# Kernel optimization log

Measured on AMD Instinct MI355X. Metric: run time of the kernel, lower is better.

## Reference

```python
import jax, jax.numpy as jnp
import numpy as np

B, D, H = 1024, 64, 512


def setup_inputs() -> dict:
    key = jax.random.key(0)
    ks = jax.random.split(key, 6)
    sc = lambda fan_in: 1.0 / np.sqrt(fan_in)
    return {
        "x_t": jax.random.normal(ks[0], (B, D), jnp.float32),
        "t": jax.random.uniform(ks[1], (B, 1), dtype=jnp.float32),
        "beta": jax.random.uniform(ks[2], (B, 1), dtype=jnp.float32),
        "W1": jax.random.normal(ks[3], (D + 1, H), jnp.float32) * sc(D + 1),
        "b1": jnp.zeros((H,), jnp.float32),
        "W2": jax.random.normal(ks[4], (H, H), jnp.float32) * sc(H),
        "b2": jnp.zeros((H,), jnp.float32),
        "W3": jax.random.normal(ks[5], (H, D), jnp.float32) * sc(H),
        "b3": jnp.zeros((D,), jnp.float32),
    }


def _score(W1, b1, W2, b2, W3, b3, x, t):
    # x: [D], t: [1] -> s: [D]; small tanh MLP score network s(x, t)
    h = jnp.tanh(jnp.concatenate([x, t]) @ W1 + b1)
    h = jnp.tanh(h @ W2 + b2)
    return h @ W3 + b3


def reference(x_t, t, beta, W1, b1, W2, b2, W3, b3):
    def per_sample(x, tt):
        s_x = lambda xx: _score(W1, b1, W2, b2, W3, b3, xx, tt)
        s_t_fn = lambda ttt: _score(W1, b1, W2, b2, W3, b3, x, ttt)

        # s_t = grad(sum(s), t): sum over output dims of ds/dt (forward-mode JVP)
        _, s_dot = jax.jvp(s_t_fn, (tt,), (jnp.ones_like(tt),))
        s_t = jnp.sum(s_dot)  # scalar per sample

        # phi(x) = div_x s + |s|^2 + <s, x>; loss term = grad_x phi (2nd order through div)
        def phi(xx):
            jac = jax.jacfwd(s_x)(xx)          # [D, D]
            div = jnp.trace(jac)
            s = s_x(xx)
            return div + jnp.sum(s * s) + jnp.dot(s, xx)

        g = jax.grad(phi)(x)  # [D]
        return s_t, g

    s_t, g = jax.vmap(per_sample)(x_t, t)  # s_t: [B], g: [B, D]
    # loss = mean_D |s_t - 0.5 * beta * grad|, shape [B, 1]
    return jnp.mean(jnp.abs(s_t[:, None] - 0.5 * beta * g), axis=1, keepdims=True)
```

## Files before the change

### kernel.cpp

```cpp
#include <hip/hip_runtime.h>
#include <math.h>


#define Bsz 1024
#define Dd  64
#define Hh  512

__global__ __launch_bounds__(256) void kpre(const float* __restrict__ W1,
                                            const float* __restrict__ W3,
                                            const float* __restrict__ W2,
                                            float* __restrict__ C,
                                            float* __restrict__ w3sum) {
  const int b = blockIdx.x;
  const int tid = threadIdx.x;
  if (b < 64) {
    __shared__ float W1s[64][68];
    __shared__ float W3s[64][68];
    const int bj = (b & 7) * 64, bl = (b >> 3) * 64;
    for (int q = 0; q < 16; q++) {
      int idx = tid + q * 256;
      int i = idx >> 6, j = idx & 63;
      W1s[i][j] = W1[i * Hh + bj + j];
    }
    for (int q = 0; q < 16; q++) {
      int idx = tid + q * 256;
      int l = idx >> 6, i = idx & 63;
      W3s[i][l] = W3[(bl + l) * Dd + i];
    }
    __syncthreads();
    const int tj = (tid >> 4) << 2, tl = (tid & 15) << 2;
    float acc[4][4] = {};
#pragma unroll 8
    for (int i = 0; i < 64; i++) {
      float4 a = *(const float4*)&W1s[i][tj];
      float4 bb = *(const float4*)&W3s[i][tl];
      float ar[4] = {a.x, a.y, a.z, a.w};
      float br[4] = {bb.x, bb.y, bb.z, bb.w};
#pragma unroll
      for (int r = 0; r < 4; r++)
#pragma unroll
        for (int c = 0; c < 4; c++) acc[r][c] += ar[r] * br[c];
    }
#pragma unroll
    for (int r = 0; r < 4; r++) {
      int j = bj + tj + r;
      float4 cv;
#pragma unroll
      for (int c = 0; c < 4; c++)
        ((float*)&cv)[c] = W2[j * Hh + bl + tl + c] * acc[r][c];
      *(float4*)&C[j * Hh + bl + tl] = cv;
    }
  } else {
#pragma unroll
    for (int r = 0; r < 2; r++) {
      int n = tid + r * 256;
      float sacc = 0.f;
#pragma unroll 4
      for (int k4 = 0; k4 < 16; k4++) {
        float4 w = *(const float4*)&W3[n * Dd + k4 * 4];
        sacc += w.x; sacc += w.y; sacc += w.z; sacc += w.w;
      }
      w3sum[n] = sacc;
    }
  }
}

__global__ __launch_bounds__(512) void kfused(const float* __restrict__ X,
                                              const float* __restrict__ tt,
                                              const float* __restrict__ beta,
                                              const float* __restrict__ W1,
                                              const float* __restrict__ b1,
                                              const float* __restrict__ W2,
                                              const float* __restrict__ b2,
                                              const float* __restrict__ W3,
                                              const float* __restrict__ b3,
                                              const float* __restrict__ C,
                                              const float* __restrict__ w3sum,
                                              float* __restrict__ out) {
  __shared__ float xs[Dd * 4], ys[Dd * 4];
  __shared__ float h1s[Hh * 4], a1s[Hh * 4], q1s[Hh * 4];
  __shared__ float h2s[Hh * 4], a2s[Hh * 4], t2s[Hh * 4], ps[Hh * 4];
  __shared__ float sts[4], tb[4], bb4[4], red[32];
  __shared__ float ph[512];

  const int tid = threadIdx.x;
  const int s0 = blockIdx.x * 4;
  const int n0 = tid;
  const int dd = tid & 63;
  const int half = (tid >> 6) & 1;
  const int ss = tid >> 7;

  if (tid < 256) {
    int sA = tid >> 6, dA = tid & 63;
    xs[dA * 4 + sA] = X[(s0 + sA) * Dd + dA];
  }
  if (tid < 4) tb[tid] = tt[s0 + tid];
  else if (tid < 8) bb4[tid - 4] = beta[s0 + tid - 4];
  __syncthreads();

  {
    float acc[4] = {};
#pragma unroll 8
    for (int k = 0; k < Dd; k++) {
      float w = W1[k * Hh + n0];
      float4 xv = *(const float4*)&xs[k * 4];
#pragma unroll
      for (int s = 0; s < 4; s++) acc[s] += w * ((float*)&xv)[s];
    }
    float wt = W1[Dd * Hh + n0];
    float bc = b1[n0];
    float4 hv, av, qv;
#pragma unroll
    for (int s = 0; s < 4; s++) {
      float z = acc[s] + tb[s] * wt + bc;
      float h = tanhf(z);
      float a = 1.f - h * h;
      ((float*)&hv)[s] = h;
      ((float*)&av)[s] = a;
      ((float*)&qv)[s] = a * wt;
    }
    *(float4*)&h1s[n0 * 4] = hv;
    *(float4*)&a1s[n0 * 4] = av;
    *(float4*)&q1s[n0 * 4] = qv;
  }
  __syncthreads();

  {
    float acc1[4] = {}, acc2[4] = {};
#pragma unroll 8
    for (int k = 0; k < Hh; k++) {
      float w = W2[k * Hh + n0];
      float4 hv = *(const float4*)&h1s[k * 4];
      float4 qv = *(const float4*)&q1s[k * 4];
#pragma unroll
      for (int s = 0; s < 4; s++) {
        acc1[s] += w * ((float*)&hv)[s];
        acc2[s] += w * ((float*)&qv)[s];
      }
    }
    float bc = b2[n0], wc = w3sum[n0];
    float stp[4];
    float4 hv, av;
#pragma unroll
    for (int s = 0; s < 4; s++) {
      float z = acc1[s] + bc;
      float h = tanhf(z);
      float a = 1.f - h * h;
      ((float*)&hv)[s] = h;
      ((float*)&av)[s] = a;
      stp[s] = a * acc2[s] * wc;
    }
    *(float4*)&h2s[n0 * 4] = hv;
    *(float4*)&a2s[n0 * 4] = av;
#pragma unroll
    for (int off = 1; off < 64; off <<= 1)
#pragma unroll
      for (int s = 0; s < 4; s++) stp[s] += __shfl_xor(stp[s], off, 64);
    if (dd == 0)
#pragma unroll
      for (int s = 0; s < 4; s++) red[(tid >> 6) * 4 + s] = stp[s];
  }
  __syncthreads();
  if (tid < 4) {
    float t = 0.f;
#pragma unroll
    for (int w = 0; w < 8; w++) t += red[w * 4 + tid];
    sts[tid] = t;
  }

  {
    float sacc = half ? 0.f : b3[dd];
    const int l0 = half * 256;
#pragma unroll 8
    for (int l = l0; l < l0 + 256; l++)
      sacc += W3[l * Dd + dd] * h2s[l * 4 + ss];
    ph[tid] = sacc;
  }
  __syncthreads();
  float sval = 0.f;
  if (half == 0) {
    sval = ph[ss * 128 + dd] + ph[ss * 128 + 64 + dd];
    ys[dd * 4 + ss] = 2.f * sval + xs[dd * 4 + ss];
  }
  __syncthreads();

  float ua[4] = {};
  {
    float r3a[4] = {};
#pragma unroll 4
    for (int k4 = 0; k4 < 16; k4++) {
      float4 w = *(const float4*)&W3[n0 * Dd + k4 * 4];
#pragma unroll
      for (int j = 0; j < 4; j++) {
        float4 yv = *(const float4*)&ys[(k4 * 4 + j) * 4];
#pragma unroll
        for (int s = 0; s < 4; s++) r3a[s] += ((float*)&w)[j] * ((float*)&yv)[s];
      }
    }
    float va[4] = {};
#pragma unroll 2
    for (int k4 = 0; k4 < 128; k4++) {
      float4 cu = *(const float4*)&C[n0 * Hh + k4 * 4];
#pragma unroll
      for (int j = 0; j < 4; j++) {
        int k = k4 * 4 + j;
        float cv = C[k * Hh + n0];
        float4 a1v = *(const float4*)&a1s[k * 4];
        float4 a2v = *(const float4*)&a2s[k * 4];
#pragma unroll
        for (int s = 0; s < 4; s++) {
          va[s] += cv * ((float*)&a1v)[s];
          ua[s] += ((float*)&cu)[j] * ((float*)&a2v)[s];
        }
      }
    }
    float4 a2r = *(const float4*)&a2s[n0 * 4];
    float4 h2r = *(const float4*)&h2s[n0 * 4];
    float4 t2v;
#pragma unroll
    for (int s = 0; s < 4; s++)
      ((float*)&t2v)[s] = ((float*)&a2r)[s] *
          (r3a[s] - 2.f * ((float*)&h2r)[s] * va[s]);
    *(float4*)&t2s[n0 * 4] = t2v;
  }
  __syncthreads();

  {
    float pa[4] = {};
#pragma unroll 2
    for (int k4 = 0; k4 < 128; k4++) {
      float4 w = *(const float4*)&W2[n0 * Hh + k4 * 4];
#pragma unroll
      for (int j = 0; j < 4; j++) {
        float4 t2v = *(const float4*)&t2s[(k4 * 4 + j) * 4];
#pragma unroll
        for (int s = 0; s < 4; s++) pa[s] += ((float*)&w)[j] * ((float*)&t2v)[s];
      }
    }
    float4 a1r = *(const float4*)&a1s[n0 * 4];
    float4 h1r = *(const float4*)&h1s[n0 * 4];
    float4 pv;
#pragma unroll
    for (int s = 0; s < 4; s++)
      ((float*)&pv)[s] = ((float*)&a1r)[s] *
          (pa[s] - 2.f * ((float*)&h1r)[s] * ua[s]);
    *(float4*)&ps[n0 * 4] = pv;
  }
  __syncthreads();

  {
    float g = (half == 0) ? sval : 0.f;
    const int j0 = half * 256;
#pragma unroll 4
    for (int j4 = 0; j4 < 64; j4++) {
      float4 w = *(const float4*)&W1[dd * Hh + j0 + j4 * 4];
#pragma unroll
      for (int j = 0; j < 4; j++)
        g += ((float*)&w)[j] * ps[(j0 + j4 * 4 + j) * 4 + ss];
    }
    ph[tid] = g;
  }
  __syncthreads();
  if (half == 0) {
    float g = ph[ss * 128 + dd] + ph[ss * 128 + 64 + dd];
    float e = fabsf(sts[ss] - 0.5f * bb4[ss] * g);
#pragma unroll
    for (int off = 32; off; off >>= 1) e += __shfl_down(e, off, 64);
    if (dd == 0) out[s0 + ss] = e * (1.f / 64.f);
  }
}

extern "C" void kernel_launch(void* const* d_in, const int* in_sizes, int n_in,
                              void* d_out, int out_size, void* d_ws, size_t ws_size,
                              hipStream_t stream) {
  const float* X    = (const float*)d_in[0];
  const float* tt   = (const float*)d_in[1];
  const float* beta = (const float*)d_in[2];
  const float* W1   = (const float*)d_in[3];
  const float* b1   = (const float*)d_in[4];
  const float* W2   = (const float*)d_in[5];
  const float* b2   = (const float*)d_in[6];
  const float* W3   = (const float*)d_in[7];
  const float* b3   = (const float*)d_in[8];
  float* out = (float*)d_out;

  float* ws  = (float*)d_ws;
  float* C   = ws;
  float* w3s = C + 262144;

  kpre<<<65, 256, 0, stream>>>(W1, W3, W2, C, w3s);
  kfused<<<256, 512, 0, stream>>>(X, tt, beta, W1, b1, W2, b2, W3, b3, C, w3s, out);
}
```

Baseline: 199.1 us.

## Pretranspose weights for row-contiguous float4 loads and halve samples per block

The precompute kernel now also writes transposed copies of C, W2, W1 and W3 into workspace. This lets every matvec in the fused kernel read a contiguous row per thread with float4 loads instead of strided column loads. The fused kernel handles 2 samples per block instead of 4, doubling the grid to 512 blocks with a higher occupancy hint. The trade-off is more workspace traffic in the precompute, and each weight byte is reused across fewer samples, so total weight reads double.

```diff
diff --git a/kernel.cpp b/kernel.cpp
--- a/kernel.cpp
+++ b/kernel.cpp
@@ -2,38 +2,40 @@
 #include <math.h>
 
 
-#define Bsz 1024
-#define Dd  64
-#define Hh  512
+#define Dd 64
+#define Hh 512
+#define S  2
 
 __global__ __launch_bounds__(256) void kpre(const float* __restrict__ W1,
                                             const float* __restrict__ W3,
                                             const float* __restrict__ W2,
                                             float* __restrict__ C,
+                                            float* __restrict__ CT,
+                                            float* __restrict__ W2T,
+                                            float* __restrict__ W1T,
+                                            float* __restrict__ W3T,
                                             float* __restrict__ w3sum) {
-  const int b = blockIdx.x;
-  const int tid = threadIdx.x;
+  const int b = blockIdx.x, tid = threadIdx.x;
+  __shared__ float sA[64][68];
+  __shared__ float sB[64][68];
+  __shared__ float sT[64][65];
   if (b < 64) {
-    __shared__ float W1s[64][68];
-    __shared__ float W3s[64][68];
     const int bj = (b & 7) * 64, bl = (b >> 3) * 64;
     for (int q = 0; q < 16; q++) {
-      int idx = tid + q * 256;
-      int i = idx >> 6, j = idx & 63;
-      W1s[i][j] = W1[i * Hh + bj + j];
-    }
-    for (int q = 0; q < 16; q++) {
-      int idx = tid + q * 256;
-      int l = idx >> 6, i = idx & 63;
-      W3s[i][l] = W3[(bl + l) * Dd + i];
+      int idx = tid + q * 256, i = idx >> 6, j = idx & 63;
+      sA[i][j] = W1[i * Hh + bj + j];
+    }
+    for (int q = 0; q < 16; q++) {
+      int idx = tid + q * 256, l = idx >> 6, i = idx & 63;
+      sB[i][l] = W3[(bl + l) * Dd + i];
     }
     __syncthreads();
     const int tj = (tid >> 4) << 2, tl = (tid & 15) << 2;
     float acc[4][4] = {};
 #pragma unroll 8
     for (int i = 0; i < 64; i++) {
-      float4 a = *(const float4*)&W1s[i][tj];
-      float4 bb = *(const float4*)&W3s[i][tl];
+      float4 a = *(const float4*)&sA[i][tj];
+      float4 bb = *(const float4*)&sB[i][tl];
       float ar[4] = {a.x, a.y, a.z, a.w};
       float br[4] = {bb.x, bb.y, bb.z, bb.w};
 #pragma unroll
@@ -41,14 +43,54 @@
 #pragma unroll
         for (int c = 0; c < 4; c++) acc[r][c] += ar[r] * br[c];
     }
+    float cv[4][4];
+#pragma unroll
+    for (int r = 0; r < 4; r++)
+#pragma unroll
+      for (int c = 0; c < 4; c++)
+        cv[r][c] = W2[(bj + tj + r) * Hh + bl + tl + c] * acc[r][c];
 #pragma unroll
     for (int r = 0; r < 4; r++) {
-      int j = bj + tj + r;
-      float4 cv;
-#pragma unroll
-      for (int c = 0; c < 4; c++)
-        ((float*)&cv)[c] = W2[j * Hh + bl + tl + c] * acc[r][c];
-      *(float4*)&C[j * Hh + bl + tl] = cv;
+      float4 o = {cv[r][0], cv[r][1], cv[r][2], cv[r][3]};
+      *(float4*)&C[(bj + tj + r) * Hh + bl + tl] = o;
+    }
+#pragma unroll
+    for (int c = 0; c < 4; c++) {
+      float4 o = {cv[0][c], cv[1][c], cv[2][c], cv[3][c]};
+      *(float4*)&CT[(bl + tl + c) * Hh + bj + tj] = o;
+    }
+  } else if (b < 128) {
+    const int t = b - 64, r0 = (t & 7) * 64, c0 = (t >> 3) * 64;
+    for (int q = 0; q < 16; q++) {
+      int idx = tid + q * 256, i = idx >> 6, j = idx & 63;
+      sT[i][j] = W2[(r0 + i) * Hh + c0 + j];
+    }
+    __syncthreads();
+    for (int q = 0; q < 16; q++) {
+      int idx = tid + q * 256, i = idx >> 6, j = idx & 63;
+      W2T[(c0 + i) * Hh + r0 + j] = sT[j][i];
+    }
+  } else if (b < 136) {
+    const int t = b - 128, c0 = t * 64;
+    for (int q = 0; q < 16; q++) {
+      int idx = tid + q * 256, i = idx >> 6, j = idx & 63;
+      sT[i][j] = W1[i * Hh + c0 + j];
+    }
+    __syncthreads();
+    for (int q = 0; q < 16; q++) {
+      int idx = tid + q * 256, i = idx >> 6, j = idx & 63;
+      W1T[(c0 + i) * Dd + j] = sT[j][i];
+    }
+  } else if (b < 144) {
+    const int t = b - 136, r0 = t * 64;
+    for (int q = 0; q < 16; q++) {
+      int idx = tid + q * 256, i = idx >> 6, j = idx & 63;
+      sT[i][j] = W3[(r0 + i) * Dd + j];
+    }
+    __syncthreads();
+    for (int q = 0; q < 16; q++) {
+      int idx = tid + q * 256, i = idx >> 6, j = idx & 63;
+      W3T[i * Hh + r0 + j] = sT[j][i];
     }
   } else {
 #pragma unroll
@@ -65,208 +107,242 @@
   }
 }
 
-__global__ __launch_bounds__(512) void kfused(const float* __restrict__ X,
-                                              const float* __restrict__ tt,
-                                              const float* __restrict__ beta,
-                                              const float* __restrict__ W1,
-                                              const float* __restrict__ b1,
-                                              const float* __restrict__ W2,
-                                              const float* __restrict__ b2,
-                                              const float* __restrict__ W3,
-                                              const float* __restrict__ b3,
-                                              const float* __restrict__ C,
-                                              const float* __restrict__ w3sum,
-                                              float* __restrict__ out) {
-  __shared__ float xs[Dd * 4], ys[Dd * 4];
-  __shared__ float h1s[Hh * 4], a1s[Hh * 4], q1s[Hh * 4];
-  __shared__ float h2s[Hh * 4], a2s[Hh * 4], t2s[Hh * 4], ps[Hh * 4];
-  __shared__ float sts[4], tb[4], bb4[4], red[32];
+__global__ __launch_bounds__(512, 4) void kfused(const float* __restrict__ X,
+                                                 const float* __restrict__ tt,
+                                                 const float* __restrict__ beta,
+                                                 const float* __restrict__ W1,
+                                                 const float* __restrict__ b1,
+                                                 const float* __restrict__ W2,
+                                                 const float* __restrict__ b2,
+                                                 const float* __restrict__ W3,
+                                                 const float* __restrict__ b3,
+                                                 const float* __restrict__ C,
+                                                 const float* __restrict__ CT,
+                                                 const float* __restrict__ W2T,
+                                                 const float* __restrict__ W1T,
+                                                 const float* __restrict__ W3T,
+                                                 const float* __restrict__ w3sum,
+                                                 float* __restrict__ out) {
+  __shared__ float xs[Dd * S], ys[Dd * S];
+  __shared__ float h1s[Hh * S], a1s[Hh * S], q1s[Hh * S];
+  __shared__ float h2s[Hh * S], a2s[Hh * S], t2s[Hh * S], ps[Hh * S];
+  __shared__ float sts[S], tb[S], bbv[S], red[8 * S];
   __shared__ float ph[512];
 
   const int tid = threadIdx.x;
-  const int s0 = blockIdx.x * 4;
+  const int s0 = blockIdx.x * S;
   const int n0 = tid;
-  const int dd = tid & 63;
-  const int half = (tid >> 6) & 1;
-  const int ss = tid >> 7;
-
-  if (tid < 256) {
+  const int ssD = tid >> 8;
+  const int qqD = (tid >> 6) & 3;
+  const int ddD = tid & 63;
+
+  if (tid < Dd * S) {
     int sA = tid >> 6, dA = tid & 63;
-    xs[dA * 4 + sA] = X[(s0 + sA) * Dd + dA];
-  }
-  if (tid < 4) tb[tid] = tt[s0 + tid];
-  else if (tid < 8) bb4[tid - 4] = beta[s0 + tid - 4];
-  __syncthreads();
-
-  {
-    float acc[4] = {};
-#pragma unroll 8
-    for (int k = 0; k < Dd; k++) {
-      float w = W1[k * Hh + n0];
-      float4 xv = *(const float4*)&xs[k * 4];
-#pragma unroll
-      for (int s = 0; s < 4; s++) acc[s] += w * ((float*)&xv)[s];
-    }
-    float wt = W1[Dd * Hh + n0];
-    float bc = b1[n0];
-    float4 hv, av, qv;
-#pragma unroll
-    for (int s = 0; s < 4; s++) {
+    xs[dA * S + sA] = X[(s0 + sA) * Dd + dA];
+  }
+  if (tid < S) tb[tid] = tt[s0 + tid];
+  if (tid >= 64 && tid < 64 + S) bbv[tid - 64] = beta[s0 + tid - 64];
+  __syncthreads();
+
+  {
+    float acc[S] = {};
+    for (int k0 = 0; k0 < Dd; k0 += 32) {
+      float4 wv[8];
+#pragma unroll
+      for (int i = 0; i < 8; i++) wv[i] = *(const float4*)&W1T[n0 * Dd + k0 + i * 4];
+#pragma unroll
+      for (int i = 0; i < 8; i++)
+#pragma unroll
+        for (int j = 0; j < 4; j++) {
+          float w = ((float*)&wv[i])[j];
+          float2 xv = *(const float2*)&xs[(k0 + i * 4 + j) * S];
+          acc[0] += w * xv.x; acc[1] += w * xv.y;
+        }
+    }
+    float wt = W1[Dd * Hh + n0], bc = b1[n0];
+    float2 hv, av, qv;
+#pragma unroll
+    for (int s = 0; s < S; s++) {
       float z = acc[s] + tb[s] * wt + bc;
       float h = tanhf(z);
       float a = 1.f - h * h;
-      ((float*)&hv)[s] = h;
-      ((float*)&av)[s] = a;
-      ((float*)&qv)[s] = a * wt;
-    }
-    *(float4*)&h1s[n0 * 4] = hv;
-    *(float4*)&a1s[n0 * 4] = av;
-    *(float4*)&q1s[n0 * 4] = qv;
-  }
-  __syncthreads();
-
-  {
-    float acc1[4] = {}, acc2[4] = {};
-#pragma unroll 8
-    for (int k = 0; k < Hh; k++) {
-      float w = W2[k * Hh + n0];
-      float4 hv = *(const float4*)&h1s[k * 4];
-      float4 qv = *(const float4*)&q1s[k * 4];
-#pragma unroll
-      for (int s = 0; s < 4; s++) {
-        acc1[s] += w * ((float*)&hv)[s];
-        acc2[s] += w * ((float*)&qv)[s];
-      }
+      ((float*)&hv)[s] = h; ((float*)&av)[s] = a; ((float*)&qv)[s] = a * wt;
+    }
+    *(float2*)&h1s[n0 * S] = hv;
+    *(float2*)&a1s[n0 * S] = av;
+    *(float2*)&q1s[n0 * S] = qv;
+  }
+  __syncthreads();
+
+  {
+    float acc1[S] = {}, acc2[S] = {};
+    for (int k0 = 0; k0 < Hh; k0 += 32) {
+      float4 wv[8];
+#pragma unroll
+      for (int i = 0; i < 8; i++) wv[i] = *(const float4*)&W2T[n0 * Hh + k0 + i * 4];
+#pragma unroll
+      for (int i = 0; i < 8; i++)
+#pragma unroll
+        for (int j = 0; j < 4; j++) {
+          int k = k0 + i * 4 + j;
+          float w = ((float*)&wv[i])[j];
+          float2 hv = *(const float2*)&h1s[k * S];
+          float2 qv = *(const float2*)&q1s[k * S];
+          acc1[0] += w * hv.x; acc1[1] += w * hv.y;
+          acc2[0] += w * qv.x; acc2[1] += w * qv.y;
+        }
     }
     float bc = b2[n0], wc = w3sum[n0];
-    float stp[4];
-    float4 hv, av;
-#pragma unroll
-    for (int s = 0; s < 4; s++) {
+    float stp[S];
+    float2 hv, av;
+#pragma unroll
+    for (int s = 0; s < S; s++) {
       float z = acc1[s] + bc;
       float h = tanhf(z);
       float a = 1.f - h * h;
-      ((float*)&hv)[s] = h;
-      ((float*)&av)[s] = a;
+      ((float*)&hv)[s] = h; ((float*)&av)[s] = a;
       stp[s] = a * acc2[s] * wc;
     }
-    *(float4*)&h2s[n0 * 4] = hv;
-    *(float4*)&a2s[n0 * 4] = av;
+    *(float2*)&h2s[n0 * S] = hv;
+    *(float2*)&a2s[n0 * S] = av;
 #pragma unroll
     for (int off = 1; off < 64; off <<= 1)
 #pragma unroll
-      for (int s = 0; s < 4; s++) stp[s] += __shfl_xor(stp[s], off, 64);
-    if (dd == 0)
-#pragma unroll
-      for (int s = 0; s < 4; s++) red[(tid >> 6) * 4 + s] = stp[s];
-  }
-  __syncthreads();
-  if (tid < 4) {
+      for (int s = 0; s < S; s++) stp[s] += __shfl_xor(stp[s], off, 64);
+    if ((tid & 63) == 0)
+#pragma unroll
+      for (int s = 0; s < S; s++) red[(tid >> 6) * S + s] = stp[s];
+  }
+  __syncthreads();
+  if (tid < S) {
     float t = 0.f;
 #pragma unroll
-    for (int w = 0; w < 8; w++) t += red[w * 4 + tid];
+    for (int w = 0; w < 8; w++) t += red[w * S + tid];
     sts[tid] = t;
   }
 
   {
-    float sacc = half ? 0.f : b3[dd];
-    const int l0 = half * 256;
-#pragma unroll 8
-    for (int l = l0; l < l0 + 256; l++)
-      sacc += W3[l * Dd + dd] * h2s[l * 4 + ss];
+    float sacc = (qqD == 0) ? b3[ddD] : 0.f;
+    const int l0 = qqD * 128;
+    for (int c0 = 0; c0 < 128; c0 += 32) {
+      float4 wv[8];
+#pragma unroll
+      for (int i = 0; i < 8; i++) wv[i] = *(const float4*)&W3T[ddD * Hh + l0 + c0 + i * 4];
+#pragma unroll
+      for (int i = 0; i < 8; i++)
+#pragma unroll
+        for (int j = 0; j < 4; j++)
+          sacc += ((float*)&wv[i])[j] * h2s[(l0 + c0 + i * 4 + j) * S + ssD];
+    }
     ph[tid] = sacc;
   }
   __syncthreads();
   float sval = 0.f;
-  if (half == 0) {
-    sval = ph[ss * 128 + dd] + ph[ss * 128 + 64 + dd];
-    ys[dd * 4 + ss] = 2.f * sval + xs[dd * 4 + ss];
-  }
-  __syncthreads();
-
-  float ua[4] = {};
-  {
-    float r3a[4] = {};
-#pragma unroll 4
-    for (int k4 = 0; k4 < 16; k4++) {
-      float4 w = *(const float4*)&W3[n0 * Dd + k4 * 4];
-#pragma unroll
-      for (int j = 0; j < 4; j++) {
-        float4 yv = *(const float4*)&ys[(k4 * 4 + j) * 4];
-#pragma unroll
-        for (int s = 0; s < 4; s++) r3a[s] += ((float*)&w)[j] * ((float*)&yv)[s];
+  if (tid < 128) {
+    int ssf = tid >> 6, ddf = tid & 63;
+    sval = ph[ssf * 256 + ddf];
+    sval += ph[ssf * 256 + 64 + ddf];
+    sval += ph[ssf * 256 + 128 + ddf];
+    sval += ph[ssf * 256 + 192 + ddf];
+    ys[ddf * S + ssf] = 2.f * sval + xs[ddf * S + ssf];
+  }
+  __syncthreads();
+
+  float ua[S] = {};
+  {
+    float r3a[S] = {};
+    for (int k0 = 0; k0 < Dd; k0 += 32) {
+      float4 wv[8];
+#pragma unroll
+      for (int i = 0; i < 8; i++) wv[i] = *(const float4*)&W3[n0 * Dd + k0 + i * 4];
+#pragma unroll
+      for (int i = 0; i < 8; i++)
+#pragma unroll
+        for (int j = 0; j < 4; j++) {
+          float w = ((float*)&wv[i])[j];
+          float2 yv = *(const float2*)&ys[(k0 + i * 4 + j) * S];
+          r3a[0] += w * yv.x; r3a[1] += w * yv.y;
+        }
+    }
+    float va[S] = {};
+    for (int k0 = 0; k0 < Hh; k0 += 16) {
+      float4 cu[4], cw[4];
+#pragma unroll
+      for (int i = 0; i < 4; i++) {
+        cu[i] = *(const float4*)&C[n0 * Hh + k0 + i * 4];
+        cw[i] = *(const float4*)&CT[n0 * Hh + k0 + i * 4];
       }
-    }
-    float va[4] = {};
-#pragma unroll 2
-    for (int k4 = 0; k4 < 128; k4++) {
-      float4 cu = *(const float4*)&C[n0 * Hh + k4 * 4];
-#pragma unroll
-      for (int j = 0; j < 4; j++) {
-        int k = k4 * 4 + j;
-        float cv = C[k * Hh + n0];
-        float4 a1v = *(const float4*)&a1s[k * 4];
-        float4 a2v = *(const float4*)&a2s[k * 4];
-#pragma unroll
-        for (int s = 0; s < 4; s++) {
-          va[s] += cv * ((float*)&a1v)[s];
-          ua[s] += ((float*)&cu)[j] * ((float*)&a2v)[s];
-        }
-      }
-    }
-    float4 a2r = *(const float4*)&a2s[n0 * 4];
-    float4 h2r = *(const float4*)&h2s[n0 * 4];
-    float4 t2v;
-#pragma unroll
-    for (int s = 0; s < 4; s++)
-      ((float*)&t2v)[s] = ((float*)&a2r)[s] *
-          (r3a[s] - 2.f * ((float*)&h2r)[s] * va[s]);
-    *(float4*)&t2s[n0 * 4] = t2v;
-  }
-  __syncthreads();
-
-  {
-    float pa[4] = {};
-#pragma unroll 2
-    for (int k4 = 0; k4 < 128; k4++) {
-      float4 w = *(const float4*)&W2[n0 * Hh + k4 * 4];
-#pragma unroll
-      for (int j = 0; j < 4; j++) {
-        float4 t2v = *(const float4*)&t2s[(k4 * 4 + j) * 4];
-#pragma unroll
-        for (int s = 0; s < 4; s++) pa[s] += ((float*)&w)[j] * ((float*)&t2v)[s];
-      }
-    }
-    float4 a1r = *(const float4*)&a1s[n0 * 4];
-    float4 h1r = *(const float4*)&h1s[n0 * 4];
-    float4 pv;
-#pragma unroll
-    for (int s = 0; s < 4; s++)
-      ((float*)&pv)[s] = ((float*)&a1r)[s] *
-          (pa[s] - 2.f * ((float*)&h1r)[s] * ua[s]);
-    *(float4*)&ps[n0 * 4] = pv;
-  }
-  __syncthreads();
-
-  {
-    float g = (half == 0) ? sval : 0.f;
-    const int j0 = half * 256;
-#pragma unroll 4
-    for (int j4 = 0; j4 < 64; j4++) {
-      float4 w = *(const float4*)&W1[dd * Hh + j0 + j4 * 4];
-#pragma unroll
-      for (int j = 0; j < 4; j++)
-        g += ((float*)&w)[j] * ps[(j0 + j4 * 4 + j) * 4 + ss];
-    }
-    ph[tid] = g;
-  }
-  __syncthreads();
-  if (half == 0) {
-    float g = ph[ss * 128 + dd] + ph[ss * 128 + 64 + dd];
-    float e = fabsf(sts[ss] - 0.5f * bb4[ss] * g);
+#pragma unroll
+      for (int i = 0; i < 4; i++)
+#pragma unroll
+        for (int j = 0; j < 4; j++) {
+          int k = k0 + i * 4 + j;
+          float2 a1v = *(const float2*)&a1s[k * S];
+          float2 a2v = *(const float2*)&a2s[k * S];
+          float u_ = ((float*)&cu[i])[j], v_ = ((float*)&cw[i])[j];
+          va[0] += v_ * a1v.x; va[1] += v_ * a1v.y;
+          ua[0] += u_ * a2v.x; ua[1] += u_ * a2v.y;
+        }
+    }
+    float2 a2r = *(const float2*)&a2s[n0 * S];
+    float2 h2r = *(const float2*)&h2s[n0 * S];
+    float2 t2v;
+    t2v.x = a2r.x * (r3a[0] - 2.f * h2r.x * va[0]);
+    t2v.y = a2r.y * (r3a[1] - 2.f * h2r.y * va[1]);
+    *(float2*)&t2s[n0 * S] = t2v;
+  }
+  __syncthreads();
+
+  {
+    float pa[S] = {};
+    for (int k0 = 0; k0 < Hh; k0 += 32) {
+      float4 wv[8];
+#pragma unroll
+      for (int i = 0; i < 8; i++) wv[i] = *(const float4*)&W2[n0 * Hh + k0 + i * 4];
+#pragma unroll
+      for (int i = 0; i < 8; i++)
+#pragma unroll
+        for (int j = 0; j < 4; j++) {
+          float w = ((float*)&wv[i])[j];
+          float2 tv = *(const float2*)&t2s[(k0 + i * 4 + j) * S];
+          pa[0] += w * tv.x; pa[1] += w * tv.y;
+        }
+    }
+    float2 a1r = *(const float2*)&a1s[n0 * S];
+    float2 h1r = *(const float2*)&h1s[n0 * S];
+    float2 pv;
+    pv.x = a1r.x * (pa[0] - 2.f * h1r.x * ua[0]);
+    pv.y = a1r.y * (pa[1] - 2.f * h1r.y * ua[1]);
+    *(float2*)&ps[n0 * S] = pv;
+  }
+  __syncthreads();
+
+  {
+    float gq = 0.f;
+    const int j0 = qqD * 128;
+    for (int c0 = 0; c0 < 128; c0 += 32) {
+      float4 wv[8];
+#pragma unroll
+      for (int i = 0; i < 8; i++) wv[i] = *(const float4*)&W1[ddD * Hh + j0 + c0 + i * 4];
+#pragma unroll
+      for (int i = 0; i < 8; i++)
+#pragma unroll
+        for (int j = 0; j < 4; j++)
+          gq += ((float*)&wv[i])[j] * ps[(j0 + c0 + i * 4 + j) * S + ssD];
+    }
+    ph[tid] = gq;
+  }
+  __syncthreads();
+  if (tid < 128) {
+    int ssf = tid >> 6, ddf = tid & 63;
+    float g = sval + ph[ssf * 256 + ddf];
+    g += ph[ssf * 256 + 64 + ddf];
+    g += ph[ssf * 256 + 128 + ddf];
+    g += ph[ssf * 256 + 192 + ddf];
+    float e = fabsf(sts[ssf] - 0.5f * bbv[ssf] * g);
 #pragma unroll
     for (int off = 32; off; off >>= 1) e += __shfl_down(e, off, 64);
-    if (dd == 0) out[s0 + ss] = e * (1.f / 64.f);
+    if (ddf == 0) out[s0 + ssf] = e * (1.f / 64.f);
   }
 }
 
@@ -284,10 +360,15 @@
   const float* b3   = (const float*)d_in[8];
   float* out = (float*)d_out;
 
-  float* ws  = (float*)d_ws;
-  float* C   = ws;
-  float* w3s = C + 262144;
-
-  kpre<<<65, 256, 0, stream>>>(W1, W3, W2, C, w3s);
-  kfused<<<256, 512, 0, stream>>>(X, tt, beta, W1, b1, W2, b2, W3, b3, C, w3s, out);
+  float* ws   = (float*)d_ws;
+  float* C    = ws;
+  float* CT   = C + 262144;
+  float* W2T  = CT + 262144;
+  float* W1T  = W2T + 262144;
+  float* W3T  = W1T + 32768;
+  float* w3s  = W3T + 32768;
+
+  kpre<<<145, 256, 0, stream>>>(W1, W3, W2, C, CT, W2T, W1T, W3T, w3s);
+  kfused<<<512, 512, 0, stream>>>(X, tt, beta, W1, b1, W2, b2, W3, b3,
+                                  C, CT, W2T, W1T, W3T, w3s, out);
 }
```

Result: slower. 392.9 us (+97.3%).

## Pre-transpose weights so fused kernel reads contiguous float4 rows per thread

Applied to the files above, without the earlier changes.

The preprocessing kernel now also writes transposed copies of C, W2, W1 and W3 into workspace. The fused kernel then reads each thread's weight row with contiguous float4 loads instead of strided scalar column loads, using macro-unrolled FMA chains. This trades coalesced scalar loads across threads for per-thread vector loads, and adds extra transpose work and workspace traffic in kpre.

```diff
diff --git a/kernel.cpp b/kernel.cpp
--- a/kernel.cpp
+++ b/kernel.cpp
@@ -2,38 +2,39 @@
 #include <math.h>
 
 
-#define Bsz 1024
-#define Dd  64
-#define Hh  512
+#define Dd 64
+#define Hh 512
 
 __global__ __launch_bounds__(256) void kpre(const float* __restrict__ W1,
                                             const float* __restrict__ W3,
                                             const float* __restrict__ W2,
                                             float* __restrict__ C,
+                                            float* __restrict__ CT,
+                                            float* __restrict__ W2T,
+                                            float* __restrict__ W1T,
+                                            float* __restrict__ W3T,
                                             float* __restrict__ w3sum) {
-  const int b = blockIdx.x;
-  const int tid = threadIdx.x;
+  const int b = blockIdx.x, tid = threadIdx.x;
+  __shared__ float sA[64][68];
+  __shared__ float sB[64][68];
+  __shared__ float sT[64][65];
   if (b < 64) {
-    __shared__ float W1s[64][68];
-    __shared__ float W3s[64][68];
     const int bj = (b & 7) * 64, bl = (b >> 3) * 64;
     for (int q = 0; q < 16; q++) {
-      int idx = tid + q * 256;
-      int i = idx >> 6, j = idx & 63;
-      W1s[i][j] = W1[i * Hh + bj + j];
-    }
-    for (int q = 0; q < 16; q++) {
-      int idx = tid + q * 256;
-      int l = idx >> 6, i = idx & 63;
-      W3s[i][l] = W3[(bl + l) * Dd + i];
+      int idx = tid + q * 256, i = idx >> 6, j = idx & 63;
+      sA[i][j] = W1[i * Hh + bj + j];
+    }
+    for (int q = 0; q < 16; q++) {
+      int idx = tid + q * 256, l = idx >> 6, i = idx & 63;
+      sB[i][l] = W3[(bl + l) * Dd + i];
     }
     __syncthreads();
     const int tj = (tid >> 4) << 2, tl = (tid & 15) << 2;
     float acc[4][4] = {};
 #pragma unroll 8
     for (int i = 0; i < 64; i++) {
-      float4 a = *(const float4*)&W1s[i][tj];
-      float4 bb = *(const float4*)&W3s[i][tl];
+      float4 a = *(const float4*)&sA[i][tj];
+      float4 bb = *(const float4*)&sB[i][tl];
       float ar[4] = {a.x, a.y, a.z, a.w};
       float br[4] = {bb.x, bb.y, bb.z, bb.w};
 #pragma unroll
@@ -41,14 +42,54 @@
 #pragma unroll
         for (int c = 0; c < 4; c++) acc[r][c] += ar[r] * br[c];
     }
+    float cv[4][4];
+#pragma unroll
+    for (int r = 0; r < 4; r++)
+#pragma unroll
+      for (int c = 0; c < 4; c++)
+        cv[r][c] = W2[(bj + tj + r) * Hh + bl + tl + c] * acc[r][c];
 #pragma unroll
     for (int r = 0; r < 4; r++) {
-      int j = bj + tj + r;
-      float4 cv;
-#pragma unroll
-      for (int c = 0; c < 4; c++)
-        ((float*)&cv)[c] = W2[j * Hh + bl + tl + c] * acc[r][c];
-      *(float4*)&C[j * Hh + bl + tl] = cv;
+      float4 o = {cv[r][0], cv[r][1], cv[r][2], cv[r][3]};
+      *(float4*)&C[(bj + tj + r) * Hh + bl + tl] = o;
+    }
+#pragma unroll
+    for (int c = 0; c < 4; c++) {
+      float4 o = {cv[0][c], cv[1][c], cv[2][c], cv[3][c]};
+      *(float4*)&CT[(bl + tl + c) * Hh + bj + tj] = o;
+    }
+  } else if (b < 128) {
+    const int t = b - 64, r0 = (t & 7) * 64, c0 = (t >> 3) * 64;
+    for (int q = 0; q < 16; q++) {
+      int idx = tid + q * 256, i = idx >> 6, j = idx & 63;
+      sT[i][j] = W2[(r0 + i) * Hh + c0 + j];
+    }
+    __syncthreads();
+    for (int q = 0; q < 16; q++) {
+      int idx = tid + q * 256, i = idx >> 6, j = idx & 63;
+      W2T[(c0 + i) * Hh + r0 + j] = sT[j][i];
+    }
+  } else if (b < 136) {
+    const int t = b - 128, c0 = t * 64;
+    for (int q = 0; q < 16; q++) {
+      int idx = tid + q * 256, i = idx >> 6, j = idx & 63;
+      sT[i][j] = W1[i * Hh + c0 + j];
+    }
+    __syncthreads();
+    for (int q = 0; q < 16; q++) {
+      int idx = tid + q * 256, i = idx >> 6, j = idx & 63;
+      W1T[(c0 + i) * Dd + j] = sT[j][i];
+    }
+  } else if (b < 144) {
+    const int t = b - 136, r0 = t * 64;
+    for (int q = 0; q < 16; q++) {
+      int idx = tid + q * 256, i = idx >> 6, j = idx & 63;
+      sT[i][j] = W3[(r0 + i) * Dd + j];
+    }
+    __syncthreads();
+    for (int q = 0; q < 16; q++) {
+      int idx = tid + q * 256, i = idx >> 6, j = idx & 63;
+      W3T[i * Hh + r0 + j] = sT[j][i];
     }
   } else {
 #pragma unroll
@@ -64,6 +105,18 @@
     }
   }
 }
+
+#define LD4(P, kb)                                   \
+  float4 w0 = *(const float4*)&(P)[(kb)];            \
+  float4 w1 = *(const float4*)&(P)[(kb) + 4];        \
+  float4 w2 = *(const float4*)&(P)[(kb) + 8];        \
+  float4 w3 = *(const float4*)&(P)[(kb) + 12];
+
+#define G16(M, kb)                                                        \
+  M(w0.x, (kb) + 0) M(w0.y, (kb) + 1) M(w0.z, (kb) + 2) M(w0.w, (kb) + 3) \
+  M(w1.x, (kb) + 4) M(w1.y, (kb) + 5) M(w1.z, (kb) + 6) M(w1.w, (kb) + 7) \
+  M(w2.x, (kb) + 8) M(w2.y, (kb) + 9) M(w2.z, (kb) + 10) M(w2.w, (kb) + 11) \
+  M(w3.x, (kb) + 12) M(w3.y, (kb) + 13) M(w3.z, (kb) + 14) M(w3.w, (kb) + 15)
 
 __global__ __launch_bounds__(512) void kfused(const float* __restrict__ X,
                                               const float* __restrict__ tt,
@@ -75,12 +128,16 @@
                                               const float* __restrict__ W3,
                                               const float* __restrict__ b3,
                                               const float* __restrict__ C,
+                                              const float* __restrict__ CT,
+                                              const float* __restrict__ W2T,
+                                              const float* __restrict__ W1T,
+                                              const float* __restrict__ W3T,
                                               const float* __restrict__ w3sum,
                                               float* __restrict__ out) {
   __shared__ float xs[Dd * 4], ys[Dd * 4];
   __shared__ float h1s[Hh * 4], a1s[Hh * 4], q1s[Hh * 4];
   __shared__ float h2s[Hh * 4], a2s[Hh * 4], t2s[Hh * 4], ps[Hh * 4];
-  __shared__ float sts[4], tb[4], bb4[4], red[32];
+  __shared__ float sts[4], tb[4], bbv[4], red[32];
   __shared__ float ph[512];
 
   const int tid = threadIdx.x;
@@ -95,29 +152,29 @@
     xs[dA * 4 + sA] = X[(s0 + sA) * Dd + dA];
   }
   if (tid < 4) tb[tid] = tt[s0 + tid];
-  else if (tid < 8) bb4[tid - 4] = beta[s0 + tid - 4];
-  __syncthreads();
-
-  {
-    float acc[4] = {};
-#pragma unroll 8
-    for (int k = 0; k < Dd; k++) {
-      float w = W1[k * Hh + n0];
-      float4 xv = *(const float4*)&xs[k * 4];
-#pragma unroll
-      for (int s = 0; s < 4; s++) acc[s] += w * ((float*)&xv)[s];
-    }
-    float wt = W1[Dd * Hh + n0];
-    float bc = b1[n0];
+  else if (tid < 8) bbv[tid - 4] = beta[s0 + tid - 4];
+  __syncthreads();
+
+  {
+    float a0 = 0.f, a1v = 0.f, a2v = 0.f, a3v = 0.f;
+    const float* Wr = &W1T[n0 * Dd];
+#define FMB(wc, kk) { float4 xv = *(const float4*)&xs[(kk) * 4]; \
+    a0 += (wc) * xv.x; a1v += (wc) * xv.y; a2v += (wc) * xv.z; a3v += (wc) * xv.w; }
+#pragma unroll
+    for (int k0 = 0; k0 < 64; k0 += 16) {
+      LD4(Wr, k0)
+      G16(FMB, k0)
+    }
+#undef FMB
+    float wt = W1[Dd * Hh + n0], bc = b1[n0];
+    float acc[4] = {a0, a1v, a2v, a3v};
     float4 hv, av, qv;
 #pragma unroll
     for (int s = 0; s < 4; s++) {
       float z = acc[s] + tb[s] * wt + bc;
       float h = tanhf(z);
       float a = 1.f - h * h;
-      ((float*)&hv)[s] = h;
-      ((float*)&av)[s] = a;
-      ((float*)&qv)[s] = a * wt;
+      ((float*)&hv)[s] = h; ((float*)&av)[s] = a; ((float*)&qv)[s] = a * wt;
     }
     *(float4*)&h1s[n0 * 4] = hv;
     *(float4*)&a1s[n0 * 4] = av;
@@ -126,19 +183,22 @@
   __syncthreads();
 
   {
-    float acc1[4] = {}, acc2[4] = {};
-#pragma unroll 8
-    for (int k = 0; k < Hh; k++) {
-      float w = W2[k * Hh + n0];
-      float4 hv = *(const float4*)&h1s[k * 4];
-      float4 qv = *(const float4*)&q1s[k * 4];
-#pragma unroll
-      for (int s = 0; s < 4; s++) {
-        acc1[s] += w * ((float*)&hv)[s];
-        acc2[s] += w * ((float*)&qv)[s];
-      }
-    }
+    float b0 = 0.f, b1a = 0.f, b2a = 0.f, b3a = 0.f;
+    float c0a = 0.f, c1a = 0.f, c2a = 0.f, c3a = 0.f;
+    const float* Wr = &W2T[n0 * Hh];
+#define FMC(wc, kk) { float4 hv_ = *(const float4*)&h1s[(kk) * 4]; \
+    float4 qv_ = *(const float4*)&q1s[(kk) * 4]; \
+    b0 += (wc) * hv_.x; b1a += (wc) * hv_.y; b2a += (wc) * hv_.z; b3a += (wc) * hv_.w; \
+    c0a += (wc) * qv_.x; c1a += (wc) * qv_.y; c2a += (wc) * qv_.z; c3a += (wc) * qv_.w; }
+#pragma unroll 2
+    for (int k0 = 0; k0 < 512; k0 += 16) {
+      LD4(Wr, k0)
+      G16(FMC, k0)
+    }
+#undef FMC
     float bc = b2[n0], wc = w3sum[n0];
+    float acc1[4] = {b0, b1a, b2a, b3a};
+    float acc2[4] = {c0a, c1a, c2a, c3a};
     float stp[4];
     float4 hv, av;
 #pragma unroll
@@ -146,8 +206,7 @@
       float z = acc1[s] + bc;
       float h = tanhf(z);
       float a = 1.f - h * h;
-      ((float*)&hv)[s] = h;
-      ((float*)&av)[s] = a;
+      ((float*)&hv)[s] = h; ((float*)&av)[s] = a;
       stp[s] = a * acc2[s] * wc;
     }
     *(float4*)&h2s[n0 * 4] = hv;
@@ -170,10 +229,15 @@
 
   {
     float sacc = half ? 0.f : b3[dd];
-    const int l0 = half * 256;
-#pragma unroll 8
-    for (int l = l0; l < l0 + 256; l++)
-      sacc += W3[l * Dd + dd] * h2s[l * 4 + ss];
+    const int hb = half * 256;
+    const float* Wr = &W3T[dd * Hh + hb];
+#define FMD(wc, ll) sacc += (wc) * h2s[(hb + (ll)) * 4 + ss];
+#pragma unroll 2
+    for (int c0 = 0; c0 < 256; c0 += 16) {
+      LD4(Wr, c0)
+      G16(FMD, c0)
+    }
+#undef FMD
     ph[tid] = sacc;
   }
   __syncthreads();
@@ -184,86 +248,88 @@
   }
   __syncthreads();
 
-  float ua[4] = {};
-  {
-    float r3a[4] = {};
-#pragma unroll 4
-    for (int k4 = 0; k4 < 16; k4++) {
-      float4 w = *(const float4*)&W3[n0 * Dd + k4 * 4];
-#pragma unroll
-      for (int j = 0; j < 4; j++) {
-        float4 yv = *(const float4*)&ys[(k4 * 4 + j) * 4];
-#pragma unroll
-        for (int s = 0; s < 4; s++) r3a[s] += ((float*)&w)[j] * ((float*)&yv)[s];
-      }
-    }
-    float va[4] = {};
-#pragma unroll 2
-    for (int k4 = 0; k4 < 128; k4++) {
-      float4 cu = *(const float4*)&C[n0 * Hh + k4 * 4];
-#pragma unroll
-      for (int j = 0; j < 4; j++) {
-        int k = k4 * 4 + j;
-        float cv = C[k * Hh + n0];
-        float4 a1v = *(const float4*)&a1s[k * 4];
-        float4 a2v = *(const float4*)&a2s[k * 4];
-#pragma unroll
-        for (int s = 0; s < 4; s++) {
-          va[s] += cv * ((float*)&a1v)[s];
-          ua[s] += ((float*)&cu)[j] * ((float*)&a2v)[s];
-        }
-      }
-    }
+  float u0 = 0.f, u1a = 0.f, u2a = 0.f, u3a = 0.f;
+  {
+    float r0 = 0.f, r1a = 0.f, r2a = 0.f, r3a = 0.f;
+    const float* Wr = &W3[n0 * Dd];
+#define FME(wc, kk) { float4 yv = *(const float4*)&ys[(kk) * 4]; \
+    r0 += (wc) * yv.x; r1a += (wc) * yv.y; r2a += (wc) * yv.z; r3a += (wc) * yv.w; }
+#pragma unroll
+    for (int k0 = 0; k0 < 64; k0 += 16) {
+      LD4(Wr, k0)
+      G16(FME, k0)
+    }
+#undef FME
+    float v0 = 0.f, v1a = 0.f, v2a = 0.f, v3a = 0.f;
+    const float* Cr = &C[n0 * Hh];
+    const float* Tr = &CT[n0 * Hh];
+#define FMU(wc, kk) { float4 av_ = *(const float4*)&a2s[(kk) * 4]; \
+    u0 += (wc) * av_.x; u1a += (wc) * av_.y; u2a += (wc) * av_.z; u3a += (wc) * av_.w; }
+#define FMV(wc, kk) { float4 av_ = *(const float4*)&a1s[(kk) * 4]; \
+    v0 += (wc) * av_.x; v1a += (wc) * av_.y; v2a += (wc) * av_.z; v3a += (wc) * av_.w; }
+#pragma unroll 2
+    for (int k0 = 0; k0 < 512; k0 += 8) {
+      float4 cu0 = *(const float4*)&Cr[k0];
+      float4 cu1 = *(const float4*)&Cr[k0 + 4];
+      float4 ct0 = *(const float4*)&Tr[k0];
+      float4 ct1 = *(const float4*)&Tr[k0 + 4];
+      FMU(cu0.x, k0 + 0) FMU(cu0.y, k0 + 1) FMU(cu0.z, k0 + 2) FMU(cu0.w, k0 + 3)
+      FMU(cu1.x, k0 + 4) FMU(cu1.y, k0 + 5) FMU(cu1.z, k0 + 6) FMU(cu1.w, k0 + 7)
+      FMV(ct0.x, k0 + 0) FMV(ct0.y, k0 + 1) FMV(ct0.z, k0 + 2) FMV(ct0.w, k0 + 3)
+      FMV(ct1.x, k0 + 4) FMV(ct1.y, k0 + 5) FMV(ct1.z, k0 + 6) FMV(ct1.w, k0 + 7)
+    }
+#undef FMU
+#undef FMV
     float4 a2r = *(const float4*)&a2s[n0 * 4];
     float4 h2r = *(const float4*)&h2s[n0 * 4];
     float4 t2v;
-#pragma unroll
-    for (int s = 0; s < 4; s++)
-      ((float*)&t2v)[s] = ((float*)&a2r)[s] *
-          (r3a[s] - 2.f * ((float*)&h2r)[s] * va[s]);
+    t2v.x = a2r.x * (r0 - 2.f * h2r.x * v0);
+    t2v.y = a2r.y * (r1a - 2.f * h2r.y * v1a);
+    t2v.z = a2r.z * (r2a - 2.f * h2r.z * v2a);
+    t2v.w = a2r.w * (r3a - 2.f * h2r.w * v3a);
     *(float4*)&t2s[n0 * 4] = t2v;
   }
   __syncthreads();
 
   {
-    float pa[4] = {};
-#pragma unroll 2
-    for (int k4 = 0; k4 < 128; k4++) {
-      float4 w = *(const float4*)&W2[n0 * Hh + k4 * 4];
-#pragma unroll
-      for (int j = 0; j < 4; j++) {
-        float4 t2v = *(const float4*)&t2s[(k4 * 4 + j) * 4];
-#pragma unroll
-        for (int s = 0; s < 4; s++) pa[s] += ((float*)&w)[j] * ((float*)&t2v)[s];
-      }
-    }
+    float p0 = 0.f, p1a = 0.f, p2a = 0.f, p3a = 0.f;
+    const float* Wr = &W2[n0 * Hh];
+#define FMF(wc, kk) { float4 tv = *(const float4*)&t2s[(kk) * 4]; \
+    p0 += (wc) * tv.x; p1a += (wc) * tv.y; p2a += (wc) * tv.z; p3a += (wc) * tv.w; }
+#pragma unroll 2
+    for (int k0 = 0; k0 < 512; k0 += 16) {
+      LD4(Wr, k0)
+      G16(FMF, k0)
+    }
+#undef FMF
     float4 a1r = *(const float4*)&a1s[n0 * 4];
     float4 h1r = *(const float4*)&h1s[n0 * 4];
     float4 pv;
-#pragma unroll
-    for (int s = 0; s < 4; s++)
-      ((float*)&pv)[s] = ((float*)&a1r)[s] *
-          (pa[s] - 2.f * ((float*)&h1r)[s] * ua[s]);
+    pv.x = a1r.x * (p0 - 2.f * h1r.x * u0);
+    pv.y = a1r.y * (p1a - 2.f * h1r.y * u1a);
+    pv.z = a1r.z * (p2a - 2.f * h1r.z * u2a);
+    pv.w = a1r.w * (p3a - 2.f * h1r.w * u3a);
     *(float4*)&ps[n0 * 4] = pv;
   }
   __syncthreads();
 
   {
-    float g = (half == 0) ? sval : 0.f;
-    const int j0 = half * 256;
-#pragma unroll 4
-    for (int j4 = 0; j4 < 64; j4++) {
-      float4 w = *(const float4*)&W1[dd * Hh + j0 + j4 * 4];
-#pragma unroll
-      for (int j = 0; j < 4; j++)
-        g += ((float*)&w)[j] * ps[(j0 + j4 * 4 + j) * 4 + ss];
-    }
-    ph[tid] = g;
+    float gq = (half == 0) ? sval : 0.f;
+    const int jb = half * 256;
+    const float* Wr = &W1[dd * Hh + jb];
+#define FMG(wc, jj) gq += (wc) * ps[(jb + (jj)) * 4 + ss];
+#pragma unroll 2
+    for (int c0 = 0; c0 < 256; c0 += 16) {
+      LD4(Wr, c0)
+      G16(FMG, c0)
+    }
+#undef FMG
+    ph[tid] = gq;
   }
   __syncthreads();
   if (half == 0) {
     float g = ph[ss * 128 + dd] + ph[ss * 128 + 64 + dd];
-    float e = fabsf(sts[ss] - 0.5f * bb4[ss] * g);
+    float e = fabsf(sts[ss] - 0.5f * bbv[ss] * g);
 #pragma unroll
     for (int off = 32; off; off >>= 1) e += __shfl_down(e, off, 64);
     if (dd == 0) out[s0 + ss] = e * (1.f / 64.f);
@@ -284,10 +350,15 @@
   const float* b3   = (const float*)d_in[8];
   float* out = (float*)d_out;
 
-  float* ws  = (float*)d_ws;
-  float* C   = ws;
-  float* w3s = C + 262144;
-
-  kpre<<<65, 256, 0, stream>>>(W1, W3, W2, C, w3s);
-  kfused<<<256, 512, 0, stream>>>(X, tt, beta, W1, b1, W2, b2, W3, b3, C, w3s, out);
+  float* ws   = (float*)d_ws;
+  float* C    = ws;
+  float* CT   = C + 262144;
+  float* W2T  = CT + 262144;
+  float* W1T  = W2T + 262144;
+  float* W3T  = W1T + 32768;
+  float* w3s  = W3T + 32768;
+
+  kpre<<<145, 256, 0, stream>>>(W1, W3, W2, C, CT, W2T, W1T, W3T, w3s);
+  kfused<<<256, 512, 0, stream>>>(X, tt, beta, W1, b1, W2, b2, W3, b3,
+                                  C, CT, W2T, W1T, W3T, w3s, out);
 }
```

After: 276.6 us. 1.39x slower.
